# Optimization experiments

Measured on AMD Instinct MI355X. Metric: run time of the kernel, lower is better.

Reference implementation:

```python
import jax, jax.numpy as jnp
import numpy as np

B, S, C, D = 128, 128, 128, 64
NQ, NT = 5000, 1441

def setup_inputs() -> dict:
    key = jax.random.key(0)
    ks = jax.random.split(key, 20)
    def xav(k, shape):
        fan_in, fan_out = shape[0], shape[1]
        lim = float(np.sqrt(6.0 / (fan_in + fan_out)))
        return jax.random.uniform(k, shape, jnp.float32, -lim, lim)
    return {
        'question_seq': jax.random.randint(ks[0], (B, S), 0, NQ),
        'correctness_seq': jax.random.randint(ks[1], (B, S), 0, 2),
        'interval_time_seq': jax.random.randint(ks[2], (B, S), 0, NT),
        'use_time_seq': jax.random.randint(ks[3], (B, S), 0, NT),
        'E_q': jax.random.normal(ks[4], (NQ, D), jnp.float32) * 0.05,
        'E_c': jax.random.normal(ks[5], (2, D), jnp.float32) * 0.05,
        'E_it': jax.random.normal(ks[6], (NT, D), jnp.float32) * 0.05,
        'E_at': jax.random.normal(ks[7], (NT, D), jnp.float32) * 0.05,
        'q_matrix': (jax.random.uniform(ks[8], (NQ, C)) < 0.1).astype(jnp.float32),
        'h0': xav(ks[9], (C, D)),
        'W1': xav(ks[10], (3 * D, D)), 'b1': jnp.zeros((D,), jnp.float32),
        'W2': xav(ks[11], (4 * D, D)), 'b2': jnp.zeros((D,), jnp.float32),
        'W3': xav(ks[12], (4 * D, D)), 'b3': jnp.zeros((D,), jnp.float32),
        'W4': xav(ks[13], (3 * D, D)), 'b4': jnp.zeros((D,), jnp.float32),
        'W5': xav(ks[14], (2 * D, D)), 'b5': jnp.zeros((D,), jnp.float32),
    }

def _lpkt_forward(question_seq, correctness_seq, interval_time_seq, use_time_seq,
                  E_q, E_c, E_it, E_at, q_matrix, h0,
                  W1, b1, W2, b2, W3, b3, W4, b4, W5, b5):
    dim_k = W1.shape[1]
    b, s = question_seq.shape
    e_emb = E_q[question_seq]            # [B,S,D]
    c_emb = E_c[correctness_seq]         # [B,S,D]
    it_emb = E_it[interval_time_seq]     # [B,S,D]
    at_emb = E_at[use_time_seq]          # [B,S,D]
    # all learning vectors (linear_1 over full sequence, as in original)
    all_learning = jnp.concatenate([e_emb, at_emb, c_emb], -1) @ W1 + b1  # [B,S,D]
    q_e_seq = q_matrix[question_seq]     # [B,S,C]

    h_pre0 = jnp.broadcast_to(h0, (b,) + h0.shape)                 # [B,C,D]
    h_tilde0 = q_e_seq[:, 0] @ h0                                  # [B,D] (h_pre is batch-replicated)
    learning0 = jnp.zeros((b, dim_k), all_learning.dtype)

    # time-major xs for t = 0 .. s-2
    xs = (jnp.swapaxes(q_e_seq[:, :-1], 0, 1),      # q_e at t
          jnp.swapaxes(q_e_seq[:, 1:], 0, 1),       # q_e at t+1
          jnp.swapaxes(it_emb[:, :-1], 0, 1),       # it at t
          jnp.swapaxes(all_learning[:, :-1], 0, 1), # learning at t
          jnp.swapaxes(e_emb[:, 1:], 0, 1))         # e embed at t+1

    def step(carry, x):
        h_pre, h_tilde_pre, learning_pre = carry
        q_e, q_e_next, it, learning, e_next = x
        x4 = jnp.concatenate([learning_pre, it, learning, h_tilde_pre], -1)   # [B,4D]
        learning_gain = jnp.tanh(x4 @ W2 + b2)
        gamma_l = jax.nn.sigmoid(x4 @ W3 + b3)
        LG = gamma_l * (learning_gain + 1.0) * 0.5                            # [B,D]
        LG_tilde = q_e[:, :, None] * LG[:, None, :]                           # [B,C,D] scatter to concepts
        c = q_e.shape[1]
        x3 = jnp.concatenate([h_pre,
                              jnp.broadcast_to(LG[:, None, :], (LG.shape[0], c, dim_k)),
                              jnp.broadcast_to(it[:, None, :], (it.shape[0], c, dim_k))], -1)
        gamma_f = jax.nn.sigmoid(x3 @ W4 + b4)                                # [B,C,D]
        h = LG_tilde + gamma_f * h_pre                                        # [B,C,D]
        h_tilde = jnp.einsum('bc,bcd->bd', q_e_next, h)                       # gather for next question
        y = jax.nn.sigmoid(jnp.concatenate([e_next, h_tilde], -1) @ W5 + b5).mean(-1)
        return (h, h_tilde, learning), y

    _, ys = jax.lax.scan(step, (h_pre0, h_tilde0, learning0), xs)  # ys: [S-1, B]
    pred = jnp.zeros((b, s), ys.dtype).at[:, 1:].set(jnp.swapaxes(ys, 0, 1))
    return pred

def reference(question_seq, correctness_seq, interval_time_seq, use_time_seq,
              E_q, E_c, E_it, E_at, q_matrix, h0,
              W1, b1, W2, b2, W3, b3, W4, b4, W5, b5):
    return _lpkt_forward(question_seq, correctness_seq, interval_time_seq, use_time_seq,
                         E_q, E_c, E_it, E_at, q_matrix, h0,
                         W1, b1, W2, b2, W3, b3, W4, b4, W5, b5)
```

## Files before the change

### kernel.cpp

```cpp
#include <hip/hip_runtime.h>
#include <hip/hip_bf16.h>


#define NB 128
#define NS 128
#define NC 128
#define ND 64
#define POS (NB*NS)

typedef __attribute__((ext_vector_type(8))) short short8;
typedef __attribute__((ext_vector_type(4))) float f32x4;
typedef __attribute__((ext_vector_type(2))) _Float16 half2_t;

__device__ __forceinline__ float rl(float v,int j){
  return __int_as_float(__builtin_amdgcn_readlane(__float_as_int(v), j));
}
__device__ __forceinline__ half2_t rlh2(half2_t v,int j){
  int x; __builtin_memcpy(&x,&v,4);
  x = __builtin_amdgcn_readlane(x,j);
  half2_t r; __builtin_memcpy(&r,&x,4); return r;
}
__device__ __forceinline__ half2_t pkrtz(float a, float b){
  auto t = __builtin_amdgcn_cvt_pkrtz(a,b);
  half2_t r; __builtin_memcpy(&r,&t,4); return r;
}
__device__ __forceinline__ float dppswap(float v){
  return __int_as_float(__builtin_amdgcn_update_dpp(0,__float_as_int(v),0xB1,0xF,0xF,true));
}
__device__ __forceinline__ float dot2h(half2_t a, half2_t b, float c){
#if __has_builtin(__builtin_amdgcn_fdot2)
  return __builtin_amdgcn_fdot2(a,b,c,false);
#else
  return fmaf((float)a[0],(float)b[0], fmaf((float)a[1],(float)b[1], c));
#endif
}

#define HBF(c, d) ((((c)<<6) + (d)) ^ (((c)&7)<<3))
#define DPP_ADD(v, CTRL) ((v) + __int_as_float(__builtin_amdgcn_update_dpp(0, __float_as_int(v), CTRL, 0xF, 0xF, true)))
#define DPP_ROWSUM(v) do { v = DPP_ADD(v,0x111); v = DPP_ADD(v,0x112); v = DPP_ADD(v,0x114); v = DPP_ADD(v,0x118); } while(0)

#define SC1 (-1.4426950408889634f)

__device__ __forceinline__ float gsig(float zp){
  return __builtin_amdgcn_rcpf(1.f + __builtin_amdgcn_exp2f(zp));
}

__global__ __launch_bounds__(64) void lpkt_pre1(
    const int* __restrict__ qseq, const int* __restrict__ cseq,
    const int* __restrict__ itseq, const int* __restrict__ atseq,
    const float* __restrict__ E_q, const float* __restrict__ E_c,
    const float* __restrict__ E_it, const float* __restrict__ E_at,
    const float* __restrict__ W1, const float* __restrict__ b1,
    const float* __restrict__ W4, const float* __restrict__ b4,
    const float* __restrict__ W5, const float* __restrict__ b5,
    float* __restrict__ AL, float* __restrict__ pre4, float* __restrict__ pre5)
{
  __shared__ float sx[4][192];
  __shared__ float sit[4][64];
  const int d = threadIdx.x;
  #pragma unroll
  for (int i = 0; i < 4; ++i) {
    int p = blockIdx.x + i*4096;
    sx[i][d]      = E_q[qseq[p]*ND + d];
    sx[i][64+d]   = E_at[atseq[p]*ND + d];
    sx[i][128+d]  = E_c[cseq[p]*ND + d];
    sit[i][d]     = E_it[itseq[p]*ND + d];
  }
  __syncthreads();
  float al[4], p4[4], p5[4];
  const float b1d = b1[d], b4d = b4[d], b5d = b5[d];
  #pragma unroll
  for (int i = 0; i < 4; ++i) { al[i] = b1d; p4[i] = b4d; p5[i] = b5d; }
  for (int k = 0; k < 192; ++k) {
    float wv = W1[k*ND + d];
    #pragma unroll
    for (int i = 0; i < 4; ++i) al[i] = fmaf(sx[i][k], wv, al[i]);
  }
  for (int k = 0; k < 64; ++k) {
    float wv4 = W4[(128+k)*ND + d];
    float wv5 = W5[k*ND + d];
    #pragma unroll
    for (int i = 0; i < 4; ++i) {
      p4[i] = fmaf(sit[i][k], wv4, p4[i]);
      p5[i] = fmaf(sx[i][k],  wv5, p5[i]);
    }
  }
  #pragma unroll
  for (int i = 0; i < 4; ++i) {
    int p = blockIdx.x + i*4096;
    AL[p*ND + d]   = al[i];
    pre4[p*ND + d] = p4[i]*SC1;
    pre5[p*ND + d] = p5[i]*SC1;
  }
}

__global__ __launch_bounds__(64) void lpkt_pre2(
    const int* __restrict__ itseq, const float* __restrict__ E_it,
    const float* __restrict__ AL,
    const float* __restrict__ W2, const float* __restrict__ b2,
    const float* __restrict__ W3, const float* __restrict__ b3,
    float* __restrict__ pre2, float* __restrict__ pre3)
{
  __shared__ float sx[4][192];
  const int d = threadIdx.x;
  int bs4[4];
  #pragma unroll
  for (int i = 0; i < 4; ++i) {
    int p = blockIdx.x + i*4064;
    int b = p / 127;
    int t = p - b*127;
    int bs = b*NS + t;
    bs4[i] = bs;
    sx[i][d]     = (t > 0) ? AL[(bs-1)*ND + d] : 0.f;
    sx[i][64+d]  = E_it[itseq[bs]*ND + d];
    sx[i][128+d] = AL[bs*ND + d];
  }
  __syncthreads();
  float a2[4], a3[4];
  const float b2d = b2[d], b3d = b3[d];
  #pragma unroll
  for (int i = 0; i < 4; ++i) { a2[i] = b2d; a3[i] = b3d; }
  for (int k = 0; k < 192; ++k) {
    float w2v = W2[k*ND + d];
    float w3v = W3[k*ND + d];
    #pragma unroll
    for (int i = 0; i < 4; ++i) {
      a2[i] = fmaf(sx[i][k], w2v, a2[i]);
      a3[i] = fmaf(sx[i][k], w3v, a3[i]);
    }
  }
  #pragma unroll
  for (int i = 0; i < 4; ++i) {
    pre2[bs4[i]*ND + d] = a2[i]*(2.f*SC1);
    pre3[bs4[i]*ND + d] = a3[i]*SC1;
  }
}

#define LOADB() do {                                                         \
  _Pragma("unroll")                                                          \
  for (int t2_=0;t2_<2;++t2_)                                                \
    _Pragma("unroll")                                                        \
    for (int k0_=0;k0_<2;++k0_)                                              \
      bfr[t2_][k0_] = *(const short8*)&sh_hbf[bfofs[t2_][k0_]];              \
} while(0)

#define MFMA8() do {                                                         \
  _Pragma("unroll")                                                          \
  for (int t2_=0;t2_<2;++t2_){                                               \
    _Pragma("unroll")                                                        \
    for (int k0_=0;k0_<2;++k0_){                                             \
      acc[0][t2_] = __builtin_amdgcn_mfma_f32_16x16x32_bf16(aW[0][k0_], bfr[t2_][k0_], acc[0][t2_],0,0,0); \
      acc[1][t2_] = __builtin_amdgcn_mfma_f32_16x16x32_bf16(aW[1][k0_], bfr[t2_][k0_], acc[1][t2_],0,0,0); \
    }                                                                        \
  }                                                                          \
} while(0)

__global__ __launch_bounds__(512)
void lpkt_seq(
    const int* __restrict__ qseq, const float* __restrict__ qmat,
    const float* __restrict__ h0,
    const float* __restrict__ W2, const float* __restrict__ W3,
    const float* __restrict__ W4, const float* __restrict__ W5,
    const float* __restrict__ pre2, const float* __restrict__ pre3,
    const float* __restrict__ pre4, const float* __restrict__ pre5,
    float* __restrict__ out)
{
  __shared__ __align__(16) unsigned short sh_hbf[NC*ND];
  __shared__ float sh_pre[32][4][64];
  __shared__ float sh_qf[32][NC];
  __shared__ float sh_htp[4][64];
  __shared__ float sh_LG[64];
  __shared__ float sh_lgp[2][64];
  __shared__ float sh_out[NS];

  const int tid = threadIdx.x;
  const int w = tid>>6, l = tid&63;
  const int g = l>>4, li = l&15;
  const int b = blockIdx.x;
  const int Wq = w & 3, mm = (w>>2)*2;

  if (w==4 || w==5) __builtin_amdgcn_s_setprio(1);

  short8 aW[2][2];
  #pragma unroll
  for (int mloc=0;mloc<2;++mloc)
    #pragma unroll
    for (int k0=0;k0<2;++k0){
      short8 v;
      #pragma unroll
      for (int j=0;j<8;++j){
        __hip_bfloat16 hb = __float2bfloat16(W4[(32*k0+8*g+j)*ND + 16*(mm+mloc)+li] * SC1);
        v[j] = *(short*)&hb;
      }
      aW[mloc][k0] = v;
    }

  half2_t wA[32], wB[32], wC[16];
  if (w==4 || w==5){
    #pragma unroll
    for (int j=0;j<32;++j){
      wA[j] = pkrtz(W2[(192+2*j)*ND + l]*(2.f*SC1), W2[(193+2*j)*ND + l]*(2.f*SC1));
      wB[j] = pkrtz(W3[(192+2*j)*ND + l]*SC1,       W3[(193+2*j)*ND + l]*SC1);
    }
    const float* pb = W4 + ((w==4)?64:96)*ND;
    #pragma unroll
    for (int j=0;j<16;++j)
      wC[j] = pkrtz(pb[(2*j)*ND + l]*SC1, pb[(2*j+1)*ND + l]*SC1);
  } else if (w==6){
    #pragma unroll
    for (int j=0;j<32;++j)
      wA[j] = pkrtz(W5[(64+2*j)*ND + l]*SC1, W5[(65+2*j)*ND + l]*SC1);
  }

  float hreg[2][2][4];
  int wofs[2][2], bfofs[2][2];
  #pragma unroll
  for (int mloc=0;mloc<2;++mloc)
    #pragma unroll
    for (int t2=0;t2<2;++t2){
      int c  = 32*Wq + 16*t2 + li;
      int d0 = 16*(mm+mloc) + 4*g;
      wofs[t2][mloc] = HBF(c, d0);
      float4 v = *(const float4*)&h0[c*ND + d0];
      hreg[mloc][t2][0]=v.x; hreg[mloc][t2][1]=v.y;
      hreg[mloc][t2][2]=v.z; hreg[mloc][t2][3]=v.w;
      __hip_bfloat162 c01 = __float22bfloat162_rn(make_float2(v.x,v.y));
      __hip_bfloat162 c23 = __float22bfloat162_rn(make_float2(v.z,v.w));
      uint2 pk; pk.x = *(unsigned*)&c01; pk.y = *(unsigned*)&c23;
      *(uint2*)&sh_hbf[wofs[t2][mloc]] = pk;
    }
  #pragma unroll
  for (int t2=0;t2<2;++t2)
    #pragma unroll
    for (int k0=0;k0<2;++k0)
      bfofs[t2][k0] = HBF(32*Wq+16*t2+li, 32*k0+8*g);

  #pragma unroll
  for (int k2=0;k2<2;++k2){
    int f4id = tid + k2*512;
    if (f4id < 17*32){
      int r = f4id >> 5, c4 = (f4id & 31)*4;
      int qrow = qseq[b*NS + r];
      float4 v = *(const float4*)&qmat[qrow*NC + c4];
      *(float4*)&sh_qf[r][c4] = v;
    }
  }
  #pragma unroll
  for (int k2=0;k2<2;++k2){
    int f4id = tid + k2*512;
    int u = f4id >> 6;
    int inner = f4id & 63;
    int s = inner >> 4, c4 = (inner & 15)*4;
    const float* ps = (s==0)?pre2:(s==1)?pre3:(s==2)?pre4:pre5;
    float4 v = *(const float4*)&ps[(size_t)(b*NS+u)*ND + c4];
    *(float4*)(&sh_pre[u][0][0] + inner*4) = v;
  }
  if (tid==0) sh_out[0] = 0.f;
  __syncthreads();

  {
    float part[2][4] = {{0.f,0.f,0.f,0.f},{0.f,0.f,0.f,0.f}};
    #pragma unroll
    for (int t2=0;t2<2;++t2){
      float qv = sh_qf[0][32*Wq+16*t2+li];
      #pragma unroll
      for (int mloc=0;mloc<2;++mloc)
        #pragma unroll
        for (int r2=0;r2<4;++r2)
          part[mloc][r2] = fmaf(qv, hreg[mloc][t2][r2], part[mloc][r2]);
    }
    #pragma unroll
    for (int mloc=0;mloc<2;++mloc)
      #pragma unroll
      for (int r2=0;r2<4;++r2){ float v=part[mloc][r2]; DPP_ROWSUM(v); part[mloc][r2]=v; }
    if (li==15){
      #pragma unroll
      for (int mloc=0;mloc<2;++mloc){
        float4 pv; pv.x=part[mloc][0]; pv.y=part[mloc][1]; pv.z=part[mloc][2]; pv.w=part[mloc][3];
        *(float4*)&sh_htp[Wq][16*(mm+mloc)+4*g] = pv;
      }
    }
  }
  __syncthreads();

  float qc0 = sh_qf[0][32*Wq+li];
  float qc1 = sh_qf[0][32*Wq+16+li];

  const float* prebase;
  { int s = l>>4;
    const float* ps = (s==0)?pre2:(s==1)?pre3:(s==2)?pre4:pre5;
    prebase = ps + (size_t)(b*NS)*ND + (l&15)*4; }

  for (int t=0; t<127; ++t){
    const int slot = t & 31, sn = (t+1) & 31;

    f32x4 acc[2][2];
    #pragma unroll
    for (int mloc=0;mloc<2;++mloc)
      #pragma unroll
      for (int t2=0;t2<2;++t2)
        acc[mloc][t2] = (f32x4){0.f,0.f,0.f,0.f};
    short8 bfr[2][2];

    if (w==4 || w==5){
      float pv2 = sh_pre[slot][0][l], pv3 = sh_pre[slot][1][l];
      float htv = (sh_htp[0][l]+sh_htp[1][l])+(sh_htp[2][l]+sh_htp[3][l]);
      half2_t hpk = pkrtz(htv, dppswap(htv));
      float a20=pv2, a21=0.f, a30=pv3, a31=0.f;
      #pragma unroll
      for (int j=0;j<32;j+=2){
        half2_t ha = rlh2(hpk, 2*j), hb = rlh2(hpk, 2*j+2);
        a20 = dot2h(ha, wA[j],   a20); a21 = dot2h(hb, wA[j+1], a21);
        a30 = dot2h(ha, wB[j],   a30); a31 = dot2h(hb, wB[j+1], a31);
      }
      float LGl = gsig(a30+a31) * gsig(a20+a21);
      half2_t LGpk = pkrtz(LGl, dppswap(LGl));
      if (w==4){
        sh_LG[l] = LGl;
        float e0 = sh_pre[slot][2][l], e1 = 0.f;
        #pragma unroll
        for (int j=0;j<16;j+=2){
          e0 = dot2h(rlh2(LGpk, 2*j),   wC[j],   e0);
          e1 = dot2h(rlh2(LGpk, 2*j+2), wC[j+1], e1);
        }
        sh_lgp[0][l] = e0+e1;
      } else {
        float e0 = 0.f, e1 = 0.f;
        #pragma unroll
        for (int j=0;j<16;j+=2){
          e0 = dot2h(rlh2(LGpk, 32+2*j),   wC[j],   e0);
          e1 = dot2h(rlh2(LGpk, 32+2*j+2), wC[j+1], e1);
        }
        sh_lgp[1][l] = e0+e1;
      }
      LOADB(); MFMA8();
    } else if (w==6){
      if (t > 0){
        float pv5 = sh_pre[slot][3][l];
        float htv = (sh_htp[0][l]+sh_htp[1][l])+(sh_htp[2][l]+sh_htp[3][l]);
        half2_t hpk = pkrtz(htv, dppswap(htv));
        float z0 = pv5, z1 = 0.f;
        #pragma unroll
        for (int j=0;j<32;j+=2){
          z0 = dot2h(rlh2(hpk, 2*j),   wA[j],   z0);
          z1 = dot2h(rlh2(hpk, 2*j+2), wA[j+1], z1);
        }
        float yv = gsig(z0+z1);
        DPP_ROWSUM(yv);
        float s = (rl(yv,15)+rl(yv,31))+(rl(yv,47)+rl(yv,63));
        if (l==0) sh_out[t] = s*(1.f/64.f);
      }
      LOADB(); MFMA8();
    } else if (w==3){
      if ((t&15)==0){
        int t0r = t+17;
        #pragma unroll
        for (int rep=0; rep<8; ++rep){
          int f4id = rep*64 + l;
          int r = t0r + (f4id>>5);
          int c4 = (f4id & 31)*4;
          if (r < NS){
            int qrow = qseq[b*NS + r];
            float4 v = *(const float4*)&qmat[qrow*NC + c4];
            *(float4*)&sh_qf[r&31][c4] = v;
          }
        }
      }
      LOADB(); MFMA8();
    } else if (w==7){
      if ((t&15)==0){
        #pragma unroll
        for (int rep=0; rep<16; ++rep){
          int u = t+16+rep;
          if (u < NS){
            float4 v = *(const float4*)&prebase[(size_t)u*ND];
            *(float4*)(&sh_pre[u&31][0][0] + l*4) = v;
          }
        }
      }
      LOADB(); MFMA8();
    } else {
      LOADB(); MFMA8();
    }
    float qn0 = sh_qf[sn][32*Wq+li];
    float qn1 = sh_qf[sn][32*Wq+16+li];
    __syncthreads();

    {
      float4 LG4[2]; float gi[2][4];
      #pragma unroll
      for (int mloc=0;mloc<2;++mloc){
        int d0 = 16*(mm+mloc)+4*g;
        LG4[mloc] = *(const float4*)&sh_LG[d0];
        float4 g0v = *(const float4*)&sh_lgp[0][d0];
        float4 g1v = *(const float4*)&sh_lgp[1][d0];
        gi[mloc][0]=g0v.x+g1v.x; gi[mloc][1]=g0v.y+g1v.y;
        gi[mloc][2]=g0v.z+g1v.z; gi[mloc][3]=g0v.w+g1v.w;
      }
      float part[2][4] = {{0.f,0.f,0.f,0.f},{0.f,0.f,0.f,0.f}};
      #pragma unroll
      for (int t2=0;t2<2;++t2){
        float qcv = t2 ? qc1 : qc0;
        float qnv = t2 ? qn1 : qn0;
        #pragma unroll
        for (int mloc=0;mloc<2;++mloc){
          float lg4a[4] = {LG4[mloc].x, LG4[mloc].y, LG4[mloc].z, LG4[mloc].w};
          float hn[4];
          #pragma unroll
          for (int r2=0;r2<4;++r2){
            float gam = gsig(acc[mloc][t2][r2] + gi[mloc][r2]);
            hn[r2] = fmaf(qcv, lg4a[r2], gam*hreg[mloc][t2][r2]);
            hreg[mloc][t2][r2] = hn[r2];
            part[mloc][r2] = fmaf(qnv, hn[r2], part[mloc][r2]);
          }
          __hip_bfloat162 c01 = __float22bfloat162_rn(make_float2(hn[0],hn[1]));
          __hip_bfloat162 c23 = __float22bfloat162_rn(make_float2(hn[2],hn[3]));
          uint2 pk; pk.x=*(unsigned*)&c01; pk.y=*(unsigned*)&c23;
          *(uint2*)&sh_hbf[wofs[t2][mloc]] = pk;
        }
      }
      #pragma unroll
      for (int mloc=0;mloc<2;++mloc)
        #pragma unroll
        for (int r2=0;r2<4;++r2){ float v=part[mloc][r2]; DPP_ROWSUM(v); part[mloc][r2]=v; }
      if (li==15){
        #pragma unroll
        for (int mloc=0;mloc<2;++mloc){
          float4 pv; pv.x=part[mloc][0]; pv.y=part[mloc][1]; pv.z=part[mloc][2]; pv.w=part[mloc][3];
          *(float4*)&sh_htp[Wq][16*(mm+mloc)+4*g] = pv;
        }
      }
      qc0 = qn0; qc1 = qn1;
    }
    __syncthreads();
  }

  if (w==6){
    float htv = (sh_htp[0][l]+sh_htp[1][l])+(sh_htp[2][l]+sh_htp[3][l]);
    half2_t hpk = pkrtz(htv, dppswap(htv));
    float z0 = sh_pre[31][3][l], z1 = 0.f;
    #pragma unroll
    for (int j=0;j<32;j+=2){
      z0 = dot2h(rlh2(hpk, 2*j),   wA[j],   z0);
      z1 = dot2h(rlh2(hpk, 2*j+2), wA[j+1], z1);
    }
    float yv = gsig(z0+z1);
    DPP_ROWSUM(yv);
    float s = (rl(yv,15)+rl(yv,31))+(rl(yv,47)+rl(yv,63));
    if (l==0) sh_out[127] = s*(1.f/64.f);
  }
  __syncthreads();
  if (tid < NS) out[b*NS + tid] = sh_out[tid];
}

extern "C" void kernel_launch(void* const* d_in, const int* in_sizes, int n_in,
                              void* d_out, int out_size, void* d_ws, size_t ws_size,
                              hipStream_t stream)
{
  const int*   qseq  = (const int*)d_in[0];
  const int*   cseq  = (const int*)d_in[1];
  const int*   itseq = (const int*)d_in[2];
  const int*   atseq = (const int*)d_in[3];
  const float* E_q   = (const float*)d_in[4];
  const float* E_c   = (const float*)d_in[5];
  const float* E_it  = (const float*)d_in[6];
  const float* E_at  = (const float*)d_in[7];
  const float* qmat  = (const float*)d_in[8];
  const float* h0    = (const float*)d_in[9];
  const float* W1    = (const float*)d_in[10];
  const float* b1    = (const float*)d_in[11];
  const float* W2    = (const float*)d_in[12];
  const float* b2    = (const float*)d_in[13];
  const float* W3    = (const float*)d_in[14];
  const float* b3    = (const float*)d_in[15];
  const float* W4    = (const float*)d_in[16];
  const float* b4    = (const float*)d_in[17];
  const float* W5    = (const float*)d_in[18];
  const float* b5    = (const float*)d_in[19];
  float* out = (float*)d_out;

  float* wsf  = (float*)d_ws;
  float* AL   = wsf;
  float* pre2 = wsf + 1*POS*ND;
  float* pre3 = wsf + 2*POS*ND;
  float* pre4 = wsf + 3*POS*ND;
  float* pre5 = wsf + 4*POS*ND;

  lpkt_pre1<<<4096, 64, 0, stream>>>(qseq, cseq, itseq, atseq,
                                     E_q, E_c, E_it, E_at,
                                     W1, b1, W4, b4, W5, b5,
                                     AL, pre4, pre5);
  lpkt_pre2<<<4064, 64, 0, stream>>>(itseq, E_it, AL, W2, b2, W3, b3, pre2, pre3);
  lpkt_seq<<<128, 512, 0, stream>>>(qseq, qmat, h0, W2, W3, W4, W5,
                                    pre2, pre3, pre4, pre5, out);
}
```

Baseline: 278.1 us.

## Specialize waves: dedicated MFMA gate waves and separate GEMV/output waves

Grows the recurrent kernel to 11 waves per block. Eight waves each own 16 concept rows and do all the gate MFMAs, while two waves compute the learning-gain GEMVs and one wave handles the output projection and prefetch. Small per-step weight matrices move from per-wave registers into swizzled shared memory and are read as uint4 vectors, which frees registers for the larger thread count. The aim is to take the serial GEMV work off the critical path of the MFMA waves. The cost is more LDS traffic and heavier barriers with 704 threads.

```diff
diff --git a/kernel.cpp b/kernel.cpp
--- a/kernel.cpp
+++ b/kernel.cpp
@@ -23,6 +23,13 @@
 __device__ __forceinline__ half2_t pkrtz(float a, float b){
   auto t = __builtin_amdgcn_cvt_pkrtz(a,b);
   half2_t r; __builtin_memcpy(&r,&t,4); return r;
+}
+__device__ __forceinline__ unsigned pkrtz_u(float a, float b){
+  auto t = __builtin_amdgcn_cvt_pkrtz(a,b);
+  unsigned r; __builtin_memcpy(&r,&t,4); return r;
+}
+__device__ __forceinline__ half2_t u2h(unsigned u){
+  half2_t r; __builtin_memcpy(&r,&u,4); return r;
 }
 __device__ __forceinline__ float dppswap(float v){
   return __int_as_float(__builtin_amdgcn_update_dpp(0,__float_as_int(v),0xB1,0xF,0xF,true));
@@ -36,6 +43,7 @@
 }
 
 #define HBF(c, d) ((((c)<<6) + (d)) ^ (((c)&7)<<3))
+#define WIDX(l_, p_) (((l_)<<5) + ((p_) ^ (((l_)&7)<<2)))
 #define DPP_ADD(v, CTRL) ((v) + __int_as_float(__builtin_amdgcn_update_dpp(0, __float_as_int(v), CTRL, 0xF, 0xF, true)))
 #define DPP_ROWSUM(v) do { v = DPP_ADD(v,0x111); v = DPP_ADD(v,0x112); v = DPP_ADD(v,0x114); v = DPP_ADD(v,0x118); } while(0)
 
@@ -136,26 +144,7 @@
   }
 }
 
-#define LOADB() do {                                                         \
-  _Pragma("unroll")                                                          \
-  for (int t2_=0;t2_<2;++t2_)                                                \
-    _Pragma("unroll")                                                        \
-    for (int k0_=0;k0_<2;++k0_)                                              \
-      bfr[t2_][k0_] = *(const short8*)&sh_hbf[bfofs[t2_][k0_]];              \
-} while(0)
-
-#define MFMA8() do {                                                         \
-  _Pragma("unroll")                                                          \
-  for (int t2_=0;t2_<2;++t2_){                                               \
-    _Pragma("unroll")                                                        \
-    for (int k0_=0;k0_<2;++k0_){                                             \
-      acc[0][t2_] = __builtin_amdgcn_mfma_f32_16x16x32_bf16(aW[0][k0_], bfr[t2_][k0_], acc[0][t2_],0,0,0); \
-      acc[1][t2_] = __builtin_amdgcn_mfma_f32_16x16x32_bf16(aW[1][k0_], bfr[t2_][k0_], acc[1][t2_],0,0,0); \
-    }                                                                        \
-  }                                                                          \
-} while(0)
-
-__global__ __launch_bounds__(512)
+__global__ __launch_bounds__(704)
 void lpkt_seq(
     const int* __restrict__ qseq, const float* __restrict__ qmat,
     const float* __restrict__ h0,
@@ -168,7 +157,11 @@
   __shared__ __align__(16) unsigned short sh_hbf[NC*ND];
   __shared__ float sh_pre[32][4][64];
   __shared__ float sh_qf[32][NC];
-  __shared__ float sh_htp[4][64];
+  __shared__ __align__(16) unsigned sh_wA[2048];
+  __shared__ __align__(16) unsigned sh_wB[2048];
+  __shared__ __align__(16) unsigned sh_wC[2048];
+  __shared__ __align__(16) unsigned sh_wy[2048];
+  __shared__ float sh_htp[8][64];
   __shared__ float sh_LG[64];
   __shared__ float sh_lgp[2][64];
   __shared__ float sh_out[NS];
@@ -177,67 +170,54 @@
   const int w = tid>>6, l = tid&63;
   const int g = l>>4, li = l&15;
   const int b = blockIdx.x;
-  const int Wq = w & 3, mm = (w>>2)*2;
-
-  if (w==4 || w==5) __builtin_amdgcn_s_setprio(1);
-
-  short8 aW[2][2];
-  #pragma unroll
-  for (int mloc=0;mloc<2;++mloc)
-    #pragma unroll
-    for (int k0=0;k0<2;++k0){
-      short8 v;
-      #pragma unroll
-      for (int j=0;j<8;++j){
-        __hip_bfloat16 hb = __float2bfloat16(W4[(32*k0+8*g+j)*ND + 16*(mm+mloc)+li] * SC1);
-        v[j] = *(short*)&hb;
-      }
-      aW[mloc][k0] = v;
-    }
-
-  half2_t wA[32], wB[32], wC[16];
-  if (w==4 || w==5){
-    #pragma unroll
-    for (int j=0;j<32;++j){
-      wA[j] = pkrtz(W2[(192+2*j)*ND + l]*(2.f*SC1), W2[(193+2*j)*ND + l]*(2.f*SC1));
-      wB[j] = pkrtz(W3[(192+2*j)*ND + l]*SC1,       W3[(193+2*j)*ND + l]*SC1);
-    }
-    const float* pb = W4 + ((w==4)?64:96)*ND;
-    #pragma unroll
-    for (int j=0;j<16;++j)
-      wC[j] = pkrtz(pb[(2*j)*ND + l]*SC1, pb[(2*j+1)*ND + l]*SC1);
-  } else if (w==6){
-    #pragma unroll
-    for (int j=0;j<32;++j)
-      wA[j] = pkrtz(W5[(64+2*j)*ND + l]*SC1, W5[(65+2*j)*ND + l]*SC1);
-  }
-
-  float hreg[2][2][4];
-  int wofs[2][2], bfofs[2][2];
-  #pragma unroll
-  for (int mloc=0;mloc<2;++mloc)
-    #pragma unroll
-    for (int t2=0;t2<2;++t2){
-      int c  = 32*Wq + 16*t2 + li;
-      int d0 = 16*(mm+mloc) + 4*g;
-      wofs[t2][mloc] = HBF(c, d0);
+
+  if (w==8 || w==9) __builtin_amdgcn_s_setprio(1);
+
+  for (int id = tid; id < 2048; id += 704){
+    int ll = id & 63, p = id >> 6;
+    int dst = WIDX(ll, p);
+    sh_wA[dst] = pkrtz_u(W2[(192+2*p)*ND+ll]*(2.f*SC1), W2[(193+2*p)*ND+ll]*(2.f*SC1));
+    sh_wB[dst] = pkrtz_u(W3[(192+2*p)*ND+ll]*SC1,       W3[(193+2*p)*ND+ll]*SC1);
+    sh_wC[dst] = pkrtz_u(W4[(64+2*p)*ND+ll]*SC1,        W4[(65+2*p)*ND+ll]*SC1);
+    sh_wy[dst] = pkrtz_u(W5[(64+2*p)*ND+ll]*SC1,        W5[(65+2*p)*ND+ll]*SC1);
+  }
+
+  short8 aW[4][2];
+  float hreg[4][4];
+  int wofs[4], bfofs[2];
+  if (w < 8){
+    #pragma unroll
+    for (int mi=0;mi<4;++mi)
+      #pragma unroll
+      for (int k0=0;k0<2;++k0){
+        short8 v;
+        #pragma unroll
+        for (int j=0;j<8;++j){
+          __hip_bfloat16 hb = __float2bfloat16(W4[(32*k0+8*g+j)*ND + 16*mi+li] * SC1);
+          v[j] = *(short*)&hb;
+        }
+        aW[mi][k0] = v;
+      }
+    int c = 16*w + li;
+    #pragma unroll
+    for (int mi=0;mi<4;++mi){
+      int d0 = 16*mi + 4*g;
+      wofs[mi] = HBF(c, d0);
       float4 v = *(const float4*)&h0[c*ND + d0];
-      hreg[mloc][t2][0]=v.x; hreg[mloc][t2][1]=v.y;
-      hreg[mloc][t2][2]=v.z; hreg[mloc][t2][3]=v.w;
+      hreg[mi][0]=v.x; hreg[mi][1]=v.y; hreg[mi][2]=v.z; hreg[mi][3]=v.w;
+      uint2 pk; pk.x = pkrtz_u(0,0);
       __hip_bfloat162 c01 = __float22bfloat162_rn(make_float2(v.x,v.y));
       __hip_bfloat162 c23 = __float22bfloat162_rn(make_float2(v.z,v.w));
-      uint2 pk; pk.x = *(unsigned*)&c01; pk.y = *(unsigned*)&c23;
-      *(uint2*)&sh_hbf[wofs[t2][mloc]] = pk;
-    }
-  #pragma unroll
-  for (int t2=0;t2<2;++t2)
+      pk.x = *(unsigned*)&c01; pk.y = *(unsigned*)&c23;
+      *(uint2*)&sh_hbf[wofs[mi]] = pk;
+    }
     #pragma unroll
     for (int k0=0;k0<2;++k0)
-      bfofs[t2][k0] = HBF(32*Wq+16*t2+li, 32*k0+8*g);
-
-  #pragma unroll
-  for (int k2=0;k2<2;++k2){
-    int f4id = tid + k2*512;
+      bfofs[k0] = HBF(c, 32*k0+8*g);
+  }
+
+  {
+    int f4id = tid;
     if (f4id < 17*32){
       int r = f4id >> 5, c4 = (f4id & 31)*4;
       int qrow = qseq[b*NS + r];
@@ -245,9 +225,7 @@
       *(float4*)&sh_qf[r][c4] = v;
     }
   }
-  #pragma unroll
-  for (int k2=0;k2<2;++k2){
-    int f4id = tid + k2*512;
+  for (int f4id = tid; f4id < 1024; f4id += 704){
     int u = f4id >> 6;
     int inner = f4id & 63;
     int s = inner >> 4, c4 = (inner & 15)*4;
@@ -258,100 +236,100 @@
   if (tid==0) sh_out[0] = 0.f;
   __syncthreads();
 
-  {
-    float part[2][4] = {{0.f,0.f,0.f,0.f},{0.f,0.f,0.f,0.f}};
-    #pragma unroll
-    for (int t2=0;t2<2;++t2){
-      float qv = sh_qf[0][32*Wq+16*t2+li];
-      #pragma unroll
-      for (int mloc=0;mloc<2;++mloc)
-        #pragma unroll
-        for (int r2=0;r2<4;++r2)
-          part[mloc][r2] = fmaf(qv, hreg[mloc][t2][r2], part[mloc][r2]);
-    }
-    #pragma unroll
-    for (int mloc=0;mloc<2;++mloc)
-      #pragma unroll
-      for (int r2=0;r2<4;++r2){ float v=part[mloc][r2]; DPP_ROWSUM(v); part[mloc][r2]=v; }
+  float qc = 0.f;
+  if (w < 8){
+    qc = sh_qf[0][16*w+li];
+    float part[4][4];
+    #pragma unroll
+    for (int mi=0;mi<4;++mi)
+      #pragma unroll
+      for (int r2=0;r2<4;++r2) part[mi][r2] = qc * hreg[mi][r2];
+    #pragma unroll
+    for (int mi=0;mi<4;++mi)
+      #pragma unroll
+      for (int r2=0;r2<4;++r2){ float v=part[mi][r2]; DPP_ROWSUM(v); part[mi][r2]=v; }
     if (li==15){
       #pragma unroll
-      for (int mloc=0;mloc<2;++mloc){
-        float4 pv; pv.x=part[mloc][0]; pv.y=part[mloc][1]; pv.z=part[mloc][2]; pv.w=part[mloc][3];
-        *(float4*)&sh_htp[Wq][16*(mm+mloc)+4*g] = pv;
-      }
-    }
-  }
-  __syncthreads();
-
-  float qc0 = sh_qf[0][32*Wq+li];
-  float qc1 = sh_qf[0][32*Wq+16+li];
-
+      for (int mi=0;mi<4;++mi){
+        float4 pv; pv.x=part[mi][0]; pv.y=part[mi][1]; pv.z=part[mi][2]; pv.w=part[mi][3];
+        *(float4*)&sh_htp[w][16*mi+4*g] = pv;
+      }
+    }
+  }
   const float* prebase;
   { int s = l>>4;
     const float* ps = (s==0)?pre2:(s==1)?pre3:(s==2)?pre4:pre5;
     prebase = ps + (size_t)(b*NS)*ND + (l&15)*4; }
-
+  __syncthreads();
+
+  f32x4 acc[4];
   for (int t=0; t<127; ++t){
     const int slot = t & 31, sn = (t+1) & 31;
 
-    f32x4 acc[2][2];
-    #pragma unroll
-    for (int mloc=0;mloc<2;++mloc)
-      #pragma unroll
-      for (int t2=0;t2<2;++t2)
-        acc[mloc][t2] = (f32x4){0.f,0.f,0.f,0.f};
-    short8 bfr[2][2];
-
-    if (w==4 || w==5){
+    if (w < 8){
+      short8 bfr[2];
+      #pragma unroll
+      for (int k0=0;k0<2;++k0)
+        bfr[k0] = *(const short8*)&sh_hbf[bfofs[k0]];
+      #pragma unroll
+      for (int mi=0;mi<4;++mi){
+        acc[mi] = (f32x4){0.f,0.f,0.f,0.f};
+        acc[mi] = __builtin_amdgcn_mfma_f32_16x16x32_bf16(aW[mi][0], bfr[0], acc[mi],0,0,0);
+        acc[mi] = __builtin_amdgcn_mfma_f32_16x16x32_bf16(aW[mi][1], bfr[1], acc[mi],0,0,0);
+      }
+    } else if (w==8 || w==9){
       float pv2 = sh_pre[slot][0][l], pv3 = sh_pre[slot][1][l];
-      float htv = (sh_htp[0][l]+sh_htp[1][l])+(sh_htp[2][l]+sh_htp[3][l]);
+      float pv4 = (w==8) ? sh_pre[slot][2][l] : 0.f;
+      float htv = ((sh_htp[0][l]+sh_htp[1][l])+(sh_htp[2][l]+sh_htp[3][l]))
+                + ((sh_htp[4][l]+sh_htp[5][l])+(sh_htp[6][l]+sh_htp[7][l]));
       half2_t hpk = pkrtz(htv, dppswap(htv));
       float a20=pv2, a21=0.f, a30=pv3, a31=0.f;
       #pragma unroll
-      for (int j=0;j<32;j+=2){
-        half2_t ha = rlh2(hpk, 2*j), hb = rlh2(hpk, 2*j+2);
-        a20 = dot2h(ha, wA[j],   a20); a21 = dot2h(hb, wA[j+1], a21);
-        a30 = dot2h(ha, wB[j],   a30); a31 = dot2h(hb, wB[j+1], a31);
+      for (int j=0;j<8;++j){
+        uint4 ua = *(const uint4*)&sh_wA[WIDX(l,4*j)];
+        uint4 ub = *(const uint4*)&sh_wB[WIDX(l,4*j)];
+        half2_t h0_ = rlh2(hpk, 8*j+0), h1_ = rlh2(hpk, 8*j+2);
+        half2_t h2_ = rlh2(hpk, 8*j+4), h3_ = rlh2(hpk, 8*j+6);
+        a20 = dot2h(h0_, u2h(ua.x), a20); a30 = dot2h(h0_, u2h(ub.x), a30);
+        a21 = dot2h(h1_, u2h(ua.y), a21); a31 = dot2h(h1_, u2h(ub.y), a31);
+        a20 = dot2h(h2_, u2h(ua.z), a20); a30 = dot2h(h2_, u2h(ub.z), a30);
+        a21 = dot2h(h3_, u2h(ua.w), a21); a31 = dot2h(h3_, u2h(ub.w), a31);
       }
       float LGl = gsig(a30+a31) * gsig(a20+a21);
+      if (w==8) sh_LG[l] = LGl;
       half2_t LGpk = pkrtz(LGl, dppswap(LGl));
-      if (w==4){
-        sh_LG[l] = LGl;
-        float e0 = sh_pre[slot][2][l], e1 = 0.f;
-        #pragma unroll
-        for (int j=0;j<16;j+=2){
-          e0 = dot2h(rlh2(LGpk, 2*j),   wC[j],   e0);
-          e1 = dot2h(rlh2(LGpk, 2*j+2), wC[j+1], e1);
-        }
-        sh_lgp[0][l] = e0+e1;
-      } else {
-        float e0 = 0.f, e1 = 0.f;
-        #pragma unroll
-        for (int j=0;j<16;j+=2){
-          e0 = dot2h(rlh2(LGpk, 32+2*j),   wC[j],   e0);
-          e1 = dot2h(rlh2(LGpk, 32+2*j+2), wC[j+1], e1);
-        }
-        sh_lgp[1][l] = e0+e1;
-      }
-      LOADB(); MFMA8();
-    } else if (w==6){
+      float e0 = pv4, e1 = 0.f;
+      const int jb = (w==8) ? 0 : 4;
+      #pragma unroll
+      for (int j=0;j<4;++j){
+        uint4 uc = *(const uint4*)&sh_wC[WIDX(l,4*(jb+j))];
+        int p0 = 8*(jb+j);
+        half2_t h0_ = rlh2(LGpk, p0+0), h1_ = rlh2(LGpk, p0+2);
+        half2_t h2_ = rlh2(LGpk, p0+4), h3_ = rlh2(LGpk, p0+6);
+        e0 = dot2h(h0_, u2h(uc.x), e0); e1 = dot2h(h1_, u2h(uc.y), e1);
+        e0 = dot2h(h2_, u2h(uc.z), e0); e1 = dot2h(h3_, u2h(uc.w), e1);
+      }
+      sh_lgp[w-8][l] = e0+e1;
+    } else {
       if (t > 0){
         float pv5 = sh_pre[slot][3][l];
-        float htv = (sh_htp[0][l]+sh_htp[1][l])+(sh_htp[2][l]+sh_htp[3][l]);
+        float htv = ((sh_htp[0][l]+sh_htp[1][l])+(sh_htp[2][l]+sh_htp[3][l]))
+                  + ((sh_htp[4][l]+sh_htp[5][l])+(sh_htp[6][l]+sh_htp[7][l]));
         half2_t hpk = pkrtz(htv, dppswap(htv));
-        float z0 = pv5, z1 = 0.f;
-        #pragma unroll
-        for (int j=0;j<32;j+=2){
-          z0 = dot2h(rlh2(hpk, 2*j),   wA[j],   z0);
-          z1 = dot2h(rlh2(hpk, 2*j+2), wA[j+1], z1);
+        float z0=pv5, z1=0.f;
+        #pragma unroll
+        for (int j=0;j<8;++j){
+          uint4 uy = *(const uint4*)&sh_wy[WIDX(l,4*j)];
+          half2_t h0_ = rlh2(hpk, 8*j+0), h1_ = rlh2(hpk, 8*j+2);
+          half2_t h2_ = rlh2(hpk, 8*j+4), h3_ = rlh2(hpk, 8*j+6);
+          z0 = dot2h(h0_, u2h(uy.x), z0); z1 = dot2h(h1_, u2h(uy.y), z1);
+          z0 = dot2h(h2_, u2h(uy.z), z0); z1 = dot2h(h3_, u2h(uy.w), z1);
         }
         float yv = gsig(z0+z1);
         DPP_ROWSUM(yv);
         float s = (rl(yv,15)+rl(yv,31))+(rl(yv,47)+rl(yv,63));
         if (l==0) sh_out[t] = s*(1.f/64.f);
       }
-      LOADB(); MFMA8();
-    } else if (w==3){
       if ((t&15)==0){
         int t0r = t+17;
         #pragma unroll
@@ -365,10 +343,6 @@
             *(float4*)&sh_qf[r&31][c4] = v;
           }
         }
-      }
-      LOADB(); MFMA8();
-    } else if (w==7){
-      if ((t&15)==0){
         #pragma unroll
         for (int rep=0; rep<16; ++rep){
           int u = t+16+rep;
@@ -378,71 +352,62 @@
           }
         }
       }
-      LOADB(); MFMA8();
-    } else {
-      LOADB(); MFMA8();
-    }
-    float qn0 = sh_qf[sn][32*Wq+li];
-    float qn1 = sh_qf[sn][32*Wq+16+li];
+    }
     __syncthreads();
 
-    {
-      float4 LG4[2]; float gi[2][4];
-      #pragma unroll
-      for (int mloc=0;mloc<2;++mloc){
-        int d0 = 16*(mm+mloc)+4*g;
-        LG4[mloc] = *(const float4*)&sh_LG[d0];
+    if (w < 8){
+      float qn = sh_qf[sn][16*w+li];
+      float part[4][4];
+      #pragma unroll
+      for (int mi=0;mi<4;++mi){
+        int d0 = 16*mi + 4*g;
+        float4 lg4 = *(const float4*)&sh_LG[d0];
         float4 g0v = *(const float4*)&sh_lgp[0][d0];
         float4 g1v = *(const float4*)&sh_lgp[1][d0];
-        gi[mloc][0]=g0v.x+g1v.x; gi[mloc][1]=g0v.y+g1v.y;
-        gi[mloc][2]=g0v.z+g1v.z; gi[mloc][3]=g0v.w+g1v.w;
-      }
-      float part[2][4] = {{0.f,0.f,0.f,0.f},{0.f,0.f,0.f,0.f}};
-      #pragma unroll
-      for (int t2=0;t2<2;++t2){
-        float qcv = t2 ? qc1 : qc0;
-        float qnv = t2 ? qn1 : qn0;
-        #pragma unroll
-        for (int mloc=0;mloc<2;++mloc){
-          float lg4a[4] = {LG4[mloc].x, LG4[mloc].y, LG4[mloc].z, LG4[mloc].w};
-          float hn[4];
-          #pragma unroll
-          for (int r2=0;r2<4;++r2){
-            float gam = gsig(acc[mloc][t2][r2] + gi[mloc][r2]);
-            hn[r2] = fmaf(qcv, lg4a[r2], gam*hreg[mloc][t2][r2]);
-            hreg[mloc][t2][r2] = hn[r2];
-            part[mloc][r2] = fmaf(qnv, hn[r2], part[mloc][r2]);
-          }
-          __hip_bfloat162 c01 = __float22bfloat162_rn(make_float2(hn[0],hn[1]));
-          __hip_bfloat162 c23 = __float22bfloat162_rn(make_float2(hn[2],hn[3]));
-          uint2 pk; pk.x=*(unsigned*)&c01; pk.y=*(unsigned*)&c23;
-          *(uint2*)&sh_hbf[wofs[t2][mloc]] = pk;
-        }
-      }
-      #pragma unroll
-      for (int mloc=0;mloc<2;++mloc)
-        #pragma unroll
-        for (int r2=0;r2<4;++r2){ float v=part[mloc][r2]; DPP_ROWSUM(v); part[mloc][r2]=v; }
+        float gi[4] = {g0v.x+g1v.x, g0v.y+g1v.y, g0v.z+g1v.z, g0v.w+g1v.w};
+        float lg[4] = {lg4.x, lg4.y, lg4.z, lg4.w};
+        float hn[4];
+        #pragma unroll
+        for (int r2=0;r2<4;++r2){
+          float gam = gsig(acc[mi][r2] + gi[r2]);
+          hn[r2] = fmaf(qc, lg[r2], gam*hreg[mi][r2]);
+          hreg[mi][r2] = hn[r2];
+          part[mi][r2] = qn * hn[r2];
+        }
+        __hip_bfloat162 c01 = __float22bfloat162_rn(make_float2(hn[0],hn[1]));
+        __hip_bfloat162 c23 = __float22bfloat162_rn(make_float2(hn[2],hn[3]));
+        uint2 pk; pk.x=*(unsigned*)&c01; pk.y=*(unsigned*)&c23;
+        *(uint2*)&sh_hbf[wofs[mi]] = pk;
+      }
+      #pragma unroll
+      for (int mi=0;mi<4;++mi)
+        #pragma unroll
+        for (int r2=0;r2<4;++r2){ float v=part[mi][r2]; DPP_ROWSUM(v); part[mi][r2]=v; }
       if (li==15){
         #pragma unroll
-        for (int mloc=0;mloc<2;++mloc){
-          float4 pv; pv.x=part[mloc][0]; pv.y=part[mloc][1]; pv.z=part[mloc][2]; pv.w=part[mloc][3];
-          *(float4*)&sh_htp[Wq][16*(mm+mloc)+4*g] = pv;
-        }
-      }
-      qc0 = qn0; qc1 = qn1;
+        for (int mi=0;mi<4;++mi){
+          float4 pv; pv.x=part[mi][0]; pv.y=part[mi][1]; pv.z=part[mi][2]; pv.w=part[mi][3];
+          *(float4*)&sh_htp[w][16*mi+4*g] = pv;
+        }
+      }
+      qc = qn;
     }
     __syncthreads();
   }
 
-  if (w==6){
-    float htv = (sh_htp[0][l]+sh_htp[1][l])+(sh_htp[2][l]+sh_htp[3][l]);
+  if (w==10){
+    float pv5 = sh_pre[31][3][l];
+    float htv = ((sh_htp[0][l]+sh_htp[1][l])+(sh_htp[2][l]+sh_htp[3][l]))
+              + ((sh_htp[4][l]+sh_htp[5][l])+(sh_htp[6][l]+sh_htp[7][l]));
     half2_t hpk = pkrtz(htv, dppswap(htv));
-    float z0 = sh_pre[31][3][l], z1 = 0.f;
-    #pragma unroll
-    for (int j=0;j<32;j+=2){
-      z0 = dot2h(rlh2(hpk, 2*j),   wA[j],   z0);
-      z1 = dot2h(rlh2(hpk, 2*j+2), wA[j+1], z1);
+    float z0=pv5, z1=0.f;
+    #pragma unroll
+    for (int j=0;j<8;++j){
+      uint4 uy = *(const uint4*)&sh_wy[WIDX(l,4*j)];
+      half2_t h0_ = rlh2(hpk, 8*j+0), h1_ = rlh2(hpk, 8*j+2);
+      half2_t h2_ = rlh2(hpk, 8*j+4), h3_ = rlh2(hpk, 8*j+6);
+      z0 = dot2h(h0_, u2h(uy.x), z0); z1 = dot2h(h1_, u2h(uy.y), z1);
+      z0 = dot2h(h2_, u2h(uy.z), z0); z1 = dot2h(h3_, u2h(uy.w), z1);
     }
     float yv = gsig(z0+z1);
     DPP_ROWSUM(yv);
@@ -491,6 +456,6 @@
                                      W1, b1, W4, b4, W5, b5,
                                      AL, pre4, pre5);
   lpkt_pre2<<<4064, 64, 0, stream>>>(itseq, E_it, AL, W2, b2, W3, b3, pre2, pre3);
-  lpkt_seq<<<128, 512, 0, stream>>>(qseq, qmat, h0, W2, W3, W4, W5,
+  lpkt_seq<<<128, 704, 0, stream>>>(qseq, qmat, h0, W2, W3, W4, W5,
                                     pre2, pre3, pre4, pre5, out);
 }
```

New measurement: 338.0 us. 21.5% more time.

## Fold LG·W4 projection into per-wave MFMA instead of two-wave dot2 pass

Applied to the files above, without the earlier changes.

Wave 4 now only computes LG and writes it as packed bf16 to shared memory. Each wave then applies the LG part of W4 with two extra bf16 MFMAs per tile, accumulating into the gamma pre-activation after the barrier. This removes wave 5's dot-product role and the sh_lgp exchange, shortening the serial critical-path work on the specialised waves. The cost is added MFMA work and latency after the sync in every wave, plus bf16 instead of fp16 precision for the LG contribution.

```diff
diff --git a/kernel.cpp b/kernel.cpp
--- a/kernel.cpp
+++ b/kernel.cpp
@@ -170,7 +170,7 @@
   __shared__ float sh_qf[32][NC];
   __shared__ float sh_htp[4][64];
   __shared__ float sh_LG[64];
-  __shared__ float sh_lgp[2][64];
+  __shared__ __align__(16) unsigned sh_LGb[32];
   __shared__ float sh_out[NS];
 
   const int tid = threadIdx.x;
@@ -179,7 +179,7 @@
   const int b = blockIdx.x;
   const int Wq = w & 3, mm = (w>>2)*2;
 
-  if (w==4 || w==5) __builtin_amdgcn_s_setprio(1);
+  if (w==4) __builtin_amdgcn_s_setprio(1);
 
   short8 aW[2][2];
   #pragma unroll
@@ -194,18 +194,27 @@
       }
       aW[mloc][k0] = v;
     }
-
-  half2_t wA[32], wB[32], wC[16];
-  if (w==4 || w==5){
+  short8 aW4b[2][2];
+  #pragma unroll
+  for (int mloc=0;mloc<2;++mloc)
+    #pragma unroll
+    for (int k0=0;k0<2;++k0){
+      short8 v;
+      #pragma unroll
+      for (int j=0;j<8;++j){
+        __hip_bfloat16 hb = __float2bfloat16(W4[(64+32*k0+8*g+j)*ND + 16*(mm+mloc)+li] * SC1);
+        v[j] = *(short*)&hb;
+      }
+      aW4b[mloc][k0] = v;
+    }
+
+  half2_t wA[32], wB[32];
+  if (w==4){
     #pragma unroll
     for (int j=0;j<32;++j){
       wA[j] = pkrtz(W2[(192+2*j)*ND + l]*(2.f*SC1), W2[(193+2*j)*ND + l]*(2.f*SC1));
       wB[j] = pkrtz(W3[(192+2*j)*ND + l]*SC1,       W3[(193+2*j)*ND + l]*SC1);
     }
-    const float* pb = W4 + ((w==4)?64:96)*ND;
-    #pragma unroll
-    for (int j=0;j<16;++j)
-      wC[j] = pkrtz(pb[(2*j)*ND + l]*SC1, pb[(2*j+1)*ND + l]*SC1);
   } else if (w==6){
     #pragma unroll
     for (int j=0;j<32;++j)
@@ -302,7 +311,7 @@
         acc[mloc][t2] = (f32x4){0.f,0.f,0.f,0.f};
     short8 bfr[2][2];
 
-    if (w==4 || w==5){
+    if (w==4){
       float pv2 = sh_pre[slot][0][l], pv3 = sh_pre[slot][1][l];
       float htv = (sh_htp[0][l]+sh_htp[1][l])+(sh_htp[2][l]+sh_htp[3][l]);
       half2_t hpk = pkrtz(htv, dppswap(htv));
@@ -314,24 +323,11 @@
         a30 = dot2h(ha, wB[j],   a30); a31 = dot2h(hb, wB[j+1], a31);
       }
       float LGl = gsig(a30+a31) * gsig(a20+a21);
-      half2_t LGpk = pkrtz(LGl, dppswap(LGl));
-      if (w==4){
-        sh_LG[l] = LGl;
-        float e0 = sh_pre[slot][2][l], e1 = 0.f;
-        #pragma unroll
-        for (int j=0;j<16;j+=2){
-          e0 = dot2h(rlh2(LGpk, 2*j),   wC[j],   e0);
-          e1 = dot2h(rlh2(LGpk, 2*j+2), wC[j+1], e1);
-        }
-        sh_lgp[0][l] = e0+e1;
-      } else {
-        float e0 = 0.f, e1 = 0.f;
-        #pragma unroll
-        for (int j=0;j<16;j+=2){
-          e0 = dot2h(rlh2(LGpk, 32+2*j),   wC[j],   e0);
-          e1 = dot2h(rlh2(LGpk, 32+2*j+2), wC[j+1], e1);
-        }
-        sh_lgp[1][l] = e0+e1;
+      sh_LG[l] = LGl;
+      float nb = dppswap(LGl);
+      if (!(l&1)){
+        __hip_bfloat162 pk = __float22bfloat162_rn(make_float2(LGl, nb));
+        sh_LGb[l>>1] = *(unsigned*)&pk;
       }
       LOADB(); MFMA8();
     } else if (w==6){
@@ -387,15 +383,25 @@
     __syncthreads();
 
     {
+      short8 lgb[2];
+      #pragma unroll
+      for (int k0=0;k0<2;++k0)
+        lgb[k0] = *(const short8*)((const char*)sh_LGb + 64*k0 + 16*g);
+      #pragma unroll
+      for (int mloc=0;mloc<2;++mloc)
+        #pragma unroll
+        for (int t2=0;t2<2;++t2){
+          acc[mloc][t2] = __builtin_amdgcn_mfma_f32_16x16x32_bf16(aW4b[mloc][0], lgb[0], acc[mloc][t2],0,0,0);
+          acc[mloc][t2] = __builtin_amdgcn_mfma_f32_16x16x32_bf16(aW4b[mloc][1], lgb[1], acc[mloc][t2],0,0,0);
+        }
+
       float4 LG4[2]; float gi[2][4];
       #pragma unroll
       for (int mloc=0;mloc<2;++mloc){
         int d0 = 16*(mm+mloc)+4*g;
         LG4[mloc] = *(const float4*)&sh_LG[d0];
-        float4 g0v = *(const float4*)&sh_lgp[0][d0];
-        float4 g1v = *(const float4*)&sh_lgp[1][d0];
-        gi[mloc][0]=g0v.x+g1v.x; gi[mloc][1]=g0v.y+g1v.y;
-        gi[mloc][2]=g0v.z+g1v.z; gi[mloc][3]=g0v.w+g1v.w;
+        float4 p4v = *(const float4*)&sh_pre[slot][2][d0];
+        gi[mloc][0]=p4v.x; gi[mloc][1]=p4v.y; gi[mloc][2]=p4v.z; gi[mloc][3]=p4v.w;
       }
       float part[2][4] = {{0.f,0.f,0.f,0.f},{0.f,0.f,0.f,0.f}};
       #pragma unroll
```

Result: no change. 273.0 us (-1.8%).
